# Kernel optimization log

Hardware: AMD Instinct MI355X
Metric: run time of the kernel (lower is better)

Reference implementation:

```python
import jax, jax.numpy as jnp
import numpy as np
from jax import lax

GS = 29          # grid_size
DW = 15          # displacement_width
DR = 0.4         # disp_range
N = GS ** 3      # 24389 control points
P = DW ** 2      # 225 in-plane displacements
WIN = (1, 1, 3, 3, 1)
ONE = (1, 1, 1, 1, 1)


def _axis(n):
    # align_corners=False pixel-center coords in [-1, 1], as torch affine_grid
    return (2.0 * jnp.arange(n, dtype=jnp.float32) + 1.0) / n - 1.0


def make_grids():
    a = _axis(GS)
    zc, yc, xc = jnp.meshgrid(a, a, a, indexing='ij')
    grid_xyz = jnp.stack([xc, yc, zc], -1).reshape(-1, 3)  # (N,3) xyz, d-major flatten
    s = DR * _axis(DW)
    A, B = jnp.meshgrid(s, s, indexing='ij')
    Z = jnp.zeros_like(A)
    sx = jnp.stack([B, A, Z], -1).reshape(-1, 3)  # z=0 plane: (s[w], s[h], 0)
    sy = jnp.stack([B, Z, A], -1).reshape(-1, 3)  # y=0 plane: (s[w], 0, s[d])
    sz = jnp.stack([Z, B, A], -1).reshape(-1, 3)  # x=0 plane: (0, s[h], s[d])
    shift_2d = jnp.stack([sx, sy, sz], axis=1)    # (P,3,3): [disp, plane, xyz]
    return grid_xyz, shift_2d


def trilerp(vol, coords, border):
    # vol (C,D,H,W); coords (...,3) normalized xyz; align_corners=False trilinear
    C, D, H, W = vol.shape
    vflat = vol.reshape(C, -1)
    x, y, z = coords[..., 0], coords[..., 1], coords[..., 2]
    ix = 0.5 * ((x + 1.0) * W - 1.0)
    iy = 0.5 * ((y + 1.0) * H - 1.0)
    iz = 0.5 * ((z + 1.0) * D - 1.0)
    x0 = jnp.floor(ix); y0 = jnp.floor(iy); z0 = jnp.floor(iz)
    fx, fy, fz = ix - x0, iy - y0, iz - z0
    x0 = x0.astype(jnp.int32); y0 = y0.astype(jnp.int32); z0 = z0.astype(jnp.int32)
    out = 0.0
    for dz in (0, 1):
        wz = fz if dz else 1.0 - fz
        zi = z0 + dz
        for dy in (0, 1):
            wy = fy if dy else 1.0 - fy
            yi = y0 + dy
            for dx in (0, 1):
                wx = fx if dx else 1.0 - fx
                xi = x0 + dx
                w = wx * wy * wz
                xc = jnp.clip(xi, 0, W - 1)
                yc = jnp.clip(yi, 0, H - 1)
                zc = jnp.clip(zi, 0, D - 1)
                if not border:  # padding_mode='zeros'
                    inb = ((xi >= 0) & (xi < W) & (yi >= 0) & (yi < H) & (zi >= 0) & (zi < D))
                    w = w * inb.astype(vol.dtype)
                idx = (zc * H + yc) * W + xc
                out = out + vflat[:, idx] * w
    return out  # (C, *coords.shape[:-1])


def pad_dh(x):
    # ReplicationPad3d((0,0,2,2,2,2)) on a 5D tensor: pad dims 2 and 3 by 2
    return jnp.pad(x, ((0, 0), (0, 0), (2, 2), (2, 2), (0, 0)), mode='edge')


def minpool(x):
    # -MaxPool3d((3,3,1))(-x)
    return -lax.reduce_window(-x, -jnp.inf, lax.max, WIN, ONE, 'VALID')


def avgpool(x):
    # AvgPool3d((3,3,1), stride=1)
    return lax.reduce_window(x, 0.0, lax.add, WIN, ONE, 'VALID') / 9.0


def grid_smooth(cost):
    # (1,N,DW,DW,3) -> two 3x3 avg passes over the 29^3 control grid (d,h axes)
    cp = cost.transpose(2, 3, 4, 0, 1).reshape(1, 3 * P, GS, GS, GS)
    cp = avgpool(avgpool(pad_dh(cp)))
    return cp.transpose(0, 2, 3, 4, 1).reshape(1, N, DW, DW, 3)


def setup_inputs() -> dict:
    key = jax.random.key(0)
    k1, k2 = jax.random.split(key)
    C, V = 8, 64
    feat00 = jax.random.normal(k1, (1, C, V, V, V), jnp.float32)
    feat50 = jax.random.normal(k2, (1, C, V, V, V), jnp.float32)
    grid_xyz, shift_2d = make_grids()
    shift_2d_min = jnp.array(jnp.broadcast_to(shift_2d[None, None], (1, N, P, 3, 3)))
    alpha = jnp.array([1.0, 0.1, 1.0, 1.0, 0.1, 5.0], jnp.float32)
    return {"feat00": feat00, "feat50": feat50, "shift_2d_min": shift_2d_min,
            "grid_xyz": grid_xyz, "shift_2d": shift_2d, "alpha": alpha}


def reference(feat00, feat50, shift_2d_min, grid_xyz, shift_2d, alpha):
    grid29 = grid_xyz.reshape(GS, GS * GS, 3)
    sm = shift_2d_min.reshape(GS, GS * GS, P, 3, 3)
    f00, f50 = feat00[0], feat50[0]

    def chunk(args):
        g, s = args                                                # (841,3), (841,P,3,3)
        mov = trilerp(f50, g[:, None, None, :] + s, border=True)   # (C,841,P,3)
        fix = trilerp(f00, g, border=False)                        # (C,841)
        ssd = jnp.sum((fix[:, :, None, None] - mov) ** 2, axis=0)  # (841,P,3)
        return alpha[1] + alpha[0] * ssd

    pdd = lax.map(chunk, (grid29, sm)).reshape(1, N, DW, DW, 3)
    cost = avgpool(minpool(pad_dh(pdd)))
    cost = alpha[4] + alpha[2] * pdd + alpha[3] * grid_smooth(cost)
    cost = avgpool(minpool(pad_dh(cost)))
    cost_avg = grid_smooth(cost).reshape(N, P, 3)
    cost_soft = jax.nn.softmax(-alpha[5] * cost_avg, axis=1)
    pred_xyz = 0.5 * jnp.einsum('npk,pkd->nd', cost_soft, shift_2d)
    return cost_soft.reshape(N, 1, DW, DW, 3), pred_xyz, cost_avg
```

## Files before the change

### kernel.cpp

```cpp
#include <hip/hip_runtime.h>
#include <math.h>

#define GS   29
#define GS2  841
#define NCP  24389
#define DW   15
#define PP   225
#define CH   675
#define CHP  676
#define CC   8
#define VV   64
#define V3   262144
#define RP   237

typedef __attribute__((ext_vector_type(8))) _Float16 half8;
typedef __attribute__((ext_vector_type(4))) _Float16 half4;
typedef __attribute__((ext_vector_type(2))) _Float16 half2v;

__device__ __forceinline__ float sv(int i) {
    return 0.4f * ((2.f * i + 1.f) * (1.f / 15.f) - 1.f);
}

__device__ __forceinline__ void paxis(float pc, int& p0, float& wA, float& wB) {
    float iu = 0.5f * ((pc + 1.f) * (float)VV - 1.f);
    float u0f = floorf(iu);
    int u0 = (int)u0f;
    p0 = min(max(u0, 0), VV - 2);
    wA = (u0 < 0) ? 1.f : ((u0 >= VV - 1) ? 0.f : (1.f - (iu - u0f)));
    wB = 1.f - wA;
}
__device__ __forceinline__ void vaxis(float pc, int& c0, int& c1, float& w0, float& w1) {
    float iv = 0.5f * ((pc + 1.f) * (float)VV - 1.f);
    float v0f = floorf(iv);
    float fv = iv - v0f;
    int v0 = (int)v0f;
    c0 = min(max(v0, 0), VV - 1);
    c1 = min(max(v0 + 1, 0), VV - 1);
    w0 = 1.f - fv; w1 = fv;
}

__device__ __forceinline__ float sample_ssd(const _Float16* __restrict__ vol,
        int p0, float wAu, float wBu,
        int c0, int c1, float wv0, float wv1,
        int e0, int e1, float ww0, float ww1,
        half8 f8) {
    half8 acc = {0, 0, 0, 0, 0, 0, 0, 0};
#define PAIR(WC, VC, WGT) {                                               \
        float fA_ = (WGT) * wAu, fB_ = (WGT) * wBu;                       \
        _Float16 hA_ = (_Float16)fA_, hB_ = (_Float16)fB_;                \
        half8 hA8 = {hA_, hA_, hA_, hA_, hA_, hA_, hA_, hA_};             \
        half8 hB8 = {hB_, hB_, hB_, hB_, hB_, hB_, hB_, hB_};             \
        const _Float16* vp = vol + (size_t)((((WC) * VV) + (VC)) * VV + p0) * 8; \
        half8 lo = *(const half8*)vp;                                     \
        half8 hi = *(const half8*)(vp + 8);                               \
        acc += hA8 * lo;                                                  \
        acc += hB8 * hi;                                                  \
    }
    PAIR(e0, c0, ww0 * wv0)
    PAIR(e0, c1, ww0 * wv1)
    PAIR(e1, c0, ww1 * wv0)
    PAIR(e1, c1, ww1 * wv1)
#undef PAIR
    half8 d8 = f8 - acc;
#if __has_builtin(__builtin_amdgcn_fdot2)
    float ssd = 0.f;
#pragma unroll
    for (int j = 0; j < 4; j++) {
        half2v d2 = {d8[2 * j], d8[2 * j + 1]};
        ssd = __builtin_amdgcn_fdot2(d2, d2, ssd, false);
    }
    return ssd;
#else
    float ssd = 0.f;
#pragma unroll
    for (int c = 0; c < 8; c++) { float dc = (float)d8[c]; ssd = fmaf(dc, dc, ssd); }
    return ssd;
#endif
}

__global__ __launch_bounds__(256) void make_vols(const float* __restrict__ in,
                                                 _Float16* __restrict__ volA,
                                                 _Float16* __restrict__ volB) {
    int v = blockIdx.x * 256 + threadIdx.x;
    if (v >= V3) return;
    int z = v >> 12, y = (v >> 6) & 63, x = v & 63;
    half8 h;
#pragma unroll
    for (int c = 0; c < CC; c++) h[c] = (_Float16)in[c * V3 + v];
    *(half8*)(volA + (size_t)v * 8) = h;
    *(half8*)(volB + (size_t)((((z << 6) | x) << 6) | y) * 8) = h;
}

__global__ __launch_bounds__(256) void pdd_pool_n(const float* __restrict__ f00,
                                                  const _Float16* __restrict__ volA,
                                                  const _Float16* __restrict__ volB,
                                                  const float* __restrict__ grid,
                                                  const float* __restrict__ alpha,
                                                  _Float16* __restrict__ pdd,
                                                  _Float16* __restrict__ pool) {
    int n = blockIdx.x;
    int tid = threadIdx.x;
    __shared__ __align__(16) _Float16 fixh[8];
    __shared__ float rowp2[3][RP];
    __shared__ float smin[3 * 289];
    __shared__ float poolv2[3][RP];

    float gx = grid[n * 3 + 0], gy = grid[n * 3 + 1], gz = grid[n * 3 + 2];

    if (tid < 8) {
        float ix = 0.5f * ((gx + 1.f) * VV - 1.f);
        float iy = 0.5f * ((gy + 1.f) * VV - 1.f);
        float iz = 0.5f * ((gz + 1.f) * VV - 1.f);
        float x0f = floorf(ix), y0f = floorf(iy), z0f = floorf(iz);
        float fx = ix - x0f, fy = iy - y0f, fz = iz - z0f;
        int x0 = (int)x0f, y0 = (int)y0f, z0 = (int)z0f;
        const float* fc = f00 + tid * V3;
        float acc = 0.f;
        for (int dz = 0; dz < 2; dz++) {
            int zi = z0 + dz; float wz = dz ? fz : 1.f - fz;
            for (int dy = 0; dy < 2; dy++) {
                int yi = y0 + dy; float wy = dy ? fy : 1.f - fy;
                for (int dx = 0; dx < 2; dx++) {
                    int xi = x0 + dx; float wx = dx ? fx : 1.f - fx;
                    if (xi >= 0 && xi < VV && yi >= 0 && yi < VV && zi >= 0 && zi < VV)
                        acc += wx * wy * wz * fc[(zi * VV + yi) * VV + xi];
                }
            }
        }
        fixh[tid] = (_Float16)acc;
    }
    if (tid >= 225 && tid < 228) {
        int k = tid - 225;
        for (int q = PP; q < RP; q++) { rowp2[k][q] = 0.f; poolv2[k][q] = 0.f; }
    }
    __syncthreads();

    if (tid < PP) {
        int p = tid;
        int h_ = p / 15, w_ = p - 15 * h_;
        float A = sv(h_), B = sv(w_);
        half8 f8 = *(const half8*)fixh;
        float a0 = alpha[0], a1 = alpha[1];

        int pu01; float wAu01, wBu01; paxis(gx + B, pu01, wAu01, wBu01);
        int pu2 ; float wAu2 , wBu2 ; paxis(gy + B, pu2 , wAu2 , wBu2 );
        int va0, va1; float wva0, wva1; vaxis(gy + A, va0, va1, wva0, wva1);
        int wa0, wa1; float wwa0, wwa1; vaxis(gz + A, wa0, wa1, wwa0, wwa1);
        int zu0, zu1; float wzu0, wzu1; vaxis(gz, zu0, zu1, wzu0, wzu1);
        int vy0, vy1; float wvy0, wvy1; vaxis(gy, vy0, vy1, wvy0, wvy1);
        int vx0, vx1; float wvx0, wvx1; vaxis(gx, vx0, vx1, wvx0, wvx1);

        float s0 = sample_ssd(volA, pu01, wAu01, wBu01, va0, va1, wva0, wva1, zu0, zu1, wzu0, wzu1, f8);
        float s1 = sample_ssd(volA, pu01, wAu01, wBu01, vy0, vy1, wvy0, wvy1, wa0, wa1, wwa0, wwa1, f8);
        float s2 = sample_ssd(volB, pu2 , wAu2 , wBu2 , vx0, vx1, wvx0, wvx1, wa0, wa1, wwa0, wwa1, f8);
        rowp2[0][p] = a1 + a0 * s0;
        rowp2[1][p] = a1 + a0 * s1;
        rowp2[2][p] = a1 + a0 * s2;
    }
    __syncthreads();

    if (tid < 255) {
        int k = tid / 85, r = tid - 85 * k;
        int a = r / 5, bc = r - 5 * a;
        int b0 = bc * 4;
        int ra = max(a - 2, 0) * 15;
        int rb = min(max(a - 1, 0), 14) * 15;
        int rc = min(a, 14) * 15;
        float cm[6];
#pragma unroll
        for (int j = 0; j < 6; j++) {
            int cj = min(max(b0 - 2 + j, 0), 14);
            float m0 = rowp2[k][ra + cj];
            float m1 = rowp2[k][rb + cj];
            float m2 = rowp2[k][rc + cj];
            cm[j] = fminf(fminf(m0, m1), m2);
        }
#pragma unroll
        for (int o = 0; o < 4; o++) {
            int b = b0 + o;
            if (b < 17) smin[k * 289 + a * 17 + b] = fminf(fminf(cm[o], cm[o + 1]), cm[o + 2]);
        }
    }
    __syncthreads();

    if (tid < 180) {
        int k = tid / 60, r = tid - 60 * k;
        int h = r >> 2, wc = r & 3;
        int w0 = wc * 4;
        const float* S = smin + k * 289;
        float cs[6];
#pragma unroll
        for (int j = 0; j < 6; j++) {
            int cj = min(w0 + j, 16);
            cs[j] = S[h * 17 + cj] + S[(h + 1) * 17 + cj] + S[(h + 2) * 17 + cj];
        }
#pragma unroll
        for (int o = 0; o < 4; o++) {
            int w = w0 + o;
            if (w < 15) poolv2[k][h * 15 + w] = (cs[o] + cs[o + 1] + cs[o + 2]) * (1.f / 9.f);
        }
    }
    __syncthreads();

    if (tid < 169) {
        int c0 = tid * 4;
        half4 hp, hq;
#pragma unroll
        for (int j = 0; j < 4; j++) {
            int i = c0 + j;
            int p = i / 3, k = i - 3 * p;
            hp[j] = (_Float16)rowp2[k][p];
            hq[j] = (_Float16)poolv2[k][p];
        }
        *(half4*)(pdd + (size_t)n * CHP + c0) = hp;
        *(half4*)(pool + (size_t)n * CHP + c0) = hq;
    }
}

__global__ __launch_bounds__(256) void gs_z4s(const _Float16* __restrict__ in,
                                              _Float16* __restrict__ out) {
    const int COLS = GS2 * 169;
    int id = blockIdx.x * 256 + threadIdx.x;
    if (id >= COLS) return;
    int seg = blockIdx.y;
    int z0 = seg * 8;
    int z1 = min(z0 + 8, GS);
    int row = id / 169, c4 = id - 169 * row;
    size_t base = (size_t)row * CHP + c4 * 4;
    const size_t ZS = (size_t)GS2 * CHP;
    const float w0 = 1.f / 9.f, w1 = 2.f / 9.f, w2 = 3.f / 9.f;

    float v0[4], v1[4], v2[4], v3[4], v4[4];
    {
        int za = max(z0 - 2, 0), zb = max(z0 - 1, 0);
        int zd = min(z0 + 1, GS - 1), ze = min(z0 + 2, GS - 1);
        half4 ha = *(const half4*)(in + base + (size_t)za * ZS);
        half4 hb = *(const half4*)(in + base + (size_t)zb * ZS);
        half4 hc = *(const half4*)(in + base + (size_t)z0 * ZS);
        half4 hd = *(const half4*)(in + base + (size_t)zd * ZS);
        half4 he = *(const half4*)(in + base + (size_t)ze * ZS);
#pragma unroll
        for (int j = 0; j < 4; j++) {
            v0[j] = (float)ha[j]; v1[j] = (float)hb[j]; v2[j] = (float)hc[j];
            v3[j] = (float)hd[j]; v4[j] = (float)he[j];
        }
    }
    for (int z = z0; z < z1; z++) {
        half4 o;
#pragma unroll
        for (int j = 0; j < 4; j++)
            o[j] = (_Float16)(w0 * (v0[j] + v4[j]) + w1 * (v1[j] + v3[j]) + w2 * v2[j]);
        *(half4*)(out + base + (size_t)z * ZS) = o;
        int zn = min(z + 3, GS - 1);
        half4 hn = *(const half4*)(in + base + (size_t)zn * ZS);
#pragma unroll
        for (int j = 0; j < 4; j++) {
            v0[j] = v1[j]; v1[j] = v2[j]; v2[j] = v3[j]; v3[j] = v4[j];
            v4[j] = (float)hn[j];
        }
    }
}

__global__ __launch_bounds__(256) void cost_pool2_y(const _Float16* __restrict__ zs,
                                                    const _Float16* __restrict__ pdd,
                                                    const float* __restrict__ alpha,
                                                    _Float16* __restrict__ pool2) {
    int n = blockIdx.x, tid = threadIdx.x;
    int x = n % GS; int zy = n / GS; int y = zy % GS; int z = zy / GS;
    __shared__ float rowp2[3][RP];
    __shared__ float smin[3 * 289];
    __shared__ float poolv2[3][RP];

    if (tid >= 225 && tid < 228) {
        int k = tid - 225;
        for (int q = PP; q < RP; q++) { rowp2[k][q] = 0.f; poolv2[k][q] = 0.f; }
    }
    if (tid < 169) {
        int c0 = tid * 4;
        float s0 = 0.f, s1 = 0.f, s2 = 0.f, s3 = 0.f;
#pragma unroll
        for (int dy = 0; dy < 5; dy++) {
            int yy = min(max(y + dy - 2, 0), GS - 1);
            size_t off = ((size_t)(z * GS + yy) * GS + x) * CHP + c0;
            float w = (3.f - fabsf((float)dy - 2.f)) * (1.f / 9.f);
            half4 hv = *(const half4*)(zs + off);
            s0 = fmaf(w, (float)hv[0], s0);
            s1 = fmaf(w, (float)hv[1], s1);
            s2 = fmaf(w, (float)hv[2], s2);
            s3 = fmaf(w, (float)hv[3], s3);
        }
        float a2 = alpha[2], a3 = alpha[3], a4 = alpha[4];
        half4 pv = *(const half4*)(pdd + (size_t)n * CHP + c0);
        float sm[4] = {s0, s1, s2, s3};
#pragma unroll
        for (int j = 0; j < 4; j++) {
            int i = c0 + j;
            if (i < CH) {
                int p = i / 3, k = i - 3 * p;
                rowp2[k][p] = a4 + a2 * (float)pv[j] + a3 * sm[j];
            }
        }
    }
    __syncthreads();

    if (tid < 255) {
        int k = tid / 85, r = tid - 85 * k;
        int a = r / 5, bc = r - 5 * a;
        int b0 = bc * 4;
        int ra = max(a - 2, 0) * 15;
        int rb = min(max(a - 1, 0), 14) * 15;
        int rc = min(a, 14) * 15;
        float cm[6];
#pragma unroll
        for (int j = 0; j < 6; j++) {
            int cj = min(max(b0 - 2 + j, 0), 14);
            float m0 = rowp2[k][ra + cj];
            float m1 = rowp2[k][rb + cj];
            float m2 = rowp2[k][rc + cj];
            cm[j] = fminf(fminf(m0, m1), m2);
        }
#pragma unroll
        for (int o = 0; o < 4; o++) {
            int b = b0 + o;
            if (b < 17) smin[k * 289 + a * 17 + b] = fminf(fminf(cm[o], cm[o + 1]), cm[o + 2]);
        }
    }
    __syncthreads();

    if (tid < 180) {
        int k = tid / 60, r = tid - 60 * k;
        int h = r >> 2, wc = r & 3;
        int w0 = wc * 4;
        const float* S = smin + k * 289;
        float cs[6];
#pragma unroll
        for (int j = 0; j < 6; j++) {
            int cj = min(w0 + j, 16);
            cs[j] = S[h * 17 + cj] + S[(h + 1) * 17 + cj] + S[(h + 2) * 17 + cj];
        }
#pragma unroll
        for (int o = 0; o < 4; o++) {
            int w = w0 + o;
            if (w < 15) poolv2[k][h * 15 + w] = (cs[o] + cs[o + 1] + cs[o + 2]) * (1.f / 9.f);
        }
    }
    __syncthreads();

    if (tid < 169) {
        int c0 = tid * 4;
        half4 hq;
#pragma unroll
        for (int j = 0; j < 4; j++) {
            int i = c0 + j;
            int p = i / 3, k = i - 3 * p;
            hq[j] = (_Float16)poolv2[k][p];
        }
        *(half4*)(pool2 + (size_t)n * CHP + c0) = hq;
    }
}

__global__ __launch_bounds__(256) void smooth_y_softmax(const _Float16* __restrict__ zs,
                                                        const float* __restrict__ alpha,
                                                        float* __restrict__ ca,
                                                        float* __restrict__ soft,
                                                        float* __restrict__ pred) {
    int n = blockIdx.x, tid = threadIdx.x;
    int x = n % GS; int zy = n / GS; int y = zy % GS; int z = zy / GS;
    int wave = tid >> 6, lane = tid & 63;
    __shared__ float vals[CHP];
    __shared__ float partial[3][3];

    if (tid < 169) {
        int c0 = tid * 4;
        float s0 = 0.f, s1 = 0.f, s2 = 0.f, s3 = 0.f;
#pragma unroll
        for (int dy = 0; dy < 5; dy++) {
            int yy = min(max(y + dy - 2, 0), GS - 1);
            size_t off = ((size_t)(z * GS + yy) * GS + x) * CHP + c0;
            float w = (3.f - fabsf((float)dy - 2.f)) * (1.f / 9.f);
            half4 hv = *(const half4*)(zs + off);
            s0 = fmaf(w, (float)hv[0], s0);
            s1 = fmaf(w, (float)hv[1], s1);
            s2 = fmaf(w, (float)hv[2], s2);
            s3 = fmaf(w, (float)hv[3], s3);
        }
        vals[c0 + 0] = s0;
        vals[c0 + 1] = s1;
        vals[c0 + 2] = s2;
        vals[c0 + 3] = s3;
    }
    __syncthreads();

    for (int i = tid; i < CH; i += 256) ca[(size_t)n * CH + i] = vals[i];
    __syncthreads();

    float a5 = alpha[5];
    if (wave < 3) {
        int k = wave;
        float v[4], e[4];
        float m = -1e30f;
#pragma unroll
        for (int j = 0; j < 4; j++) {
            int p = lane + 64 * j;
            v[j] = (p < PP) ? -a5 * vals[p * 3 + k] : -1e30f;
            m = fmaxf(m, v[j]);
        }
#pragma unroll
        for (int o = 32; o > 0; o >>= 1) m = fmaxf(m, __shfl_xor(m, o));
        float sum = 0.f;
#pragma unroll
        for (int j = 0; j < 4; j++) {
            int p = lane + 64 * j;
            e[j] = (p < PP) ? __expf(v[j] - m) : 0.f;
            sum += e[j];
        }
#pragma unroll
        for (int o = 32; o > 0; o >>= 1) sum += __shfl_xor(sum, o);
        float inv = 1.f / sum;
        float px = 0.f, py = 0.f, pz = 0.f;
#pragma unroll
        for (int j = 0; j < 4; j++) {
            int p = lane + 64 * j;
            if (p < PP) {
                float s = e[j] * inv;
                vals[p * 3 + k] = s;
                int h_ = p / 15, w_ = p - 15 * h_;
                float A = sv(h_), B = sv(w_);
                if (k == 0)      { px += s * B; py += s * A; }
                else if (k == 1) { px += s * B; pz += s * A; }
                else             { py += s * B; pz += s * A; }
            }
        }
#pragma unroll
        for (int o = 32; o > 0; o >>= 1) {
            px += __shfl_xor(px, o);
            py += __shfl_xor(py, o);
            pz += __shfl_xor(pz, o);
        }
        if (lane == 0) { partial[k][0] = px; partial[k][1] = py; partial[k][2] = pz; }
    }
    __syncthreads();
    if (tid < 3) pred[(size_t)n * 3 + tid] = 0.5f * (partial[0][tid] + partial[1][tid] + partial[2][tid]);
    for (int i = tid; i < CH; i += 256) soft[(size_t)n * CH + i] = vals[i];
}

extern "C" void kernel_launch(void* const* d_in, const int* in_sizes, int n_in,
                              void* d_out, int out_size, void* d_ws, size_t ws_size,
                              hipStream_t stream) {
    const float* f00   = (const float*)d_in[0];
    const float* f50   = (const float*)d_in[1];
    const float* grid  = (const float*)d_in[3];
    const float* alpha = (const float*)d_in[5];

    float* out0 = (float*)d_out;
    float* out1 = out0 + (size_t)NCP * CH;
    float* out2 = out1 + (size_t)NCP * 3;

    char* ws = (char*)d_ws;
    _Float16* volA = (_Float16*)ws;
    _Float16* volB = volA + (size_t)V3 * 8;
    _Float16* H0 = volB + (size_t)V3 * 8;
    _Float16* H1 = H0 + (size_t)NCP * CHP;
    _Float16* H2 = H1 + (size_t)NCP * CHP;

    make_vols<<<(V3 + 255) / 256, 256, 0, stream>>>(f50, volA, volB);

    pdd_pool_n<<<NCP, 256, 0, stream>>>(f00, volA, volB, grid, alpha, H0, H1);

    const int COLS = GS2 * 169;
    const int gbz = (COLS + 255) / 256;
    dim3 gz(gbz, 4);

    gs_z4s<<<gz, 256, 0, stream>>>(H1, H2);
    cost_pool2_y<<<NCP, 256, 0, stream>>>(H2, H0, alpha, H1);

    gs_z4s<<<gz, 256, 0, stream>>>(H1, H2);
    smooth_y_softmax<<<NCP, 256, 0, stream>>>(H2, alpha, out2, out0, out1);
}
```

Before: 484.3 us.

## Fuse tail kernels into one persistent kernel with software grid barriers

Replaces the four tail launches (z-smooth, cost/pool, z-smooth, y-smooth+softmax) with a single persistent kernel of 1024 blocks that loops over work and synchronises phases through atomic-counter grid barriers. This targets launch overhead and inter-kernel drain gaps. It relies on all 1024 blocks being co-resident, since otherwise the spin barrier deadlocks. It also adds a memset for the barrier counters and per-block serial looping over control points.

New measurement: 1.280 ms. 164% more time.

```diff
diff --git a/kernel.cpp b/kernel.cpp
--- a/kernel.cpp
+++ b/kernel.cpp
@@ -1,5 +1,6 @@
 #include <hip/hip_runtime.h>
 #include <math.h>
+#include <stdint.h>
 
 #define GS   29
 #define GS2  841
@@ -12,6 +13,8 @@
 #define VV   64
 #define V3   262144
 #define RP   237
+#define COLS (GS2 * 169)
+#define NBT  1024
 
 typedef __attribute__((ext_vector_type(8))) _Float16 half8;
 typedef __attribute__((ext_vector_type(4))) _Float16 half4;
@@ -217,231 +220,260 @@
     }
 }
 
-__global__ __launch_bounds__(256) void gs_z4s(const _Float16* __restrict__ in,
-                                              _Float16* __restrict__ out) {
-    const int COLS = GS2 * 169;
-    int id = blockIdx.x * 256 + threadIdx.x;
-    if (id >= COLS) return;
-    int seg = blockIdx.y;
-    int z0 = seg * 8;
-    int z1 = min(z0 + 8, GS);
-    int row = id / 169, c4 = id - 169 * row;
-    size_t base = (size_t)row * CHP + c4 * 4;
+
+__device__ __forceinline__ void gridbar(unsigned* bar, int idx, unsigned nb) {
+    __syncthreads();
+    __threadfence();
+    if (threadIdx.x == 0) {
+        unsigned* c = bar + idx * 16;
+        atomicAdd(c, 1u);
+        while (__hip_atomic_load(c, __ATOMIC_ACQUIRE, __HIP_MEMORY_SCOPE_AGENT) < nb) {
+            __builtin_amdgcn_s_sleep(8);
+        }
+    }
+    __syncthreads();
+    __threadfence();
+}
+
+__device__ __forceinline__ void zsmooth_phase(const _Float16* __restrict__ in,
+                                              _Float16* __restrict__ out, int nthreads) {
     const size_t ZS = (size_t)GS2 * CHP;
     const float w0 = 1.f / 9.f, w1 = 2.f / 9.f, w2 = 3.f / 9.f;
-
-    float v0[4], v1[4], v2[4], v3[4], v4[4];
-    {
-        int za = max(z0 - 2, 0), zb = max(z0 - 1, 0);
-        int zd = min(z0 + 1, GS - 1), ze = min(z0 + 2, GS - 1);
-        half4 ha = *(const half4*)(in + base + (size_t)za * ZS);
-        half4 hb = *(const half4*)(in + base + (size_t)zb * ZS);
-        half4 hc = *(const half4*)(in + base + (size_t)z0 * ZS);
-        half4 hd = *(const half4*)(in + base + (size_t)zd * ZS);
-        half4 he = *(const half4*)(in + base + (size_t)ze * ZS);
-#pragma unroll
-        for (int j = 0; j < 4; j++) {
-            v0[j] = (float)ha[j]; v1[j] = (float)hb[j]; v2[j] = (float)hc[j];
-            v3[j] = (float)hd[j]; v4[j] = (float)he[j];
-        }
-    }
-    for (int z = z0; z < z1; z++) {
-        half4 o;
-#pragma unroll
-        for (int j = 0; j < 4; j++)
-            o[j] = (_Float16)(w0 * (v0[j] + v4[j]) + w1 * (v1[j] + v3[j]) + w2 * v2[j]);
-        *(half4*)(out + base + (size_t)z * ZS) = o;
-        int zn = min(z + 3, GS - 1);
-        half4 hn = *(const half4*)(in + base + (size_t)zn * ZS);
-#pragma unroll
-        for (int j = 0; j < 4; j++) {
-            v0[j] = v1[j]; v1[j] = v2[j]; v2[j] = v3[j]; v3[j] = v4[j];
-            v4[j] = (float)hn[j];
-        }
-    }
-}
-
-__global__ __launch_bounds__(256) void cost_pool2_y(const _Float16* __restrict__ zs,
-                                                    const _Float16* __restrict__ pdd,
-                                                    const float* __restrict__ alpha,
-                                                    _Float16* __restrict__ pool2) {
-    int n = blockIdx.x, tid = threadIdx.x;
-    int x = n % GS; int zy = n / GS; int y = zy % GS; int z = zy / GS;
+    const int TOT = COLS * 4;
+    for (int w = blockIdx.x * 256 + threadIdx.x; w < TOT; w += nthreads) {
+        int seg = w / COLS; int id = w - seg * COLS;
+        int z0 = seg * 8;
+        int z1 = min(z0 + 8, GS);
+        int row = id / 169, c4 = id - 169 * row;
+        size_t base = (size_t)row * CHP + c4 * 4;
+
+        float v0[4], v1[4], v2[4], v3[4], v4[4];
+        {
+            int za = max(z0 - 2, 0), zb = max(z0 - 1, 0);
+            int zd = min(z0 + 1, GS - 1), ze = min(z0 + 2, GS - 1);
+            half4 ha = *(const half4*)(in + base + (size_t)za * ZS);
+            half4 hb = *(const half4*)(in + base + (size_t)zb * ZS);
+            half4 hc = *(const half4*)(in + base + (size_t)z0 * ZS);
+            half4 hd = *(const half4*)(in + base + (size_t)zd * ZS);
+            half4 he = *(const half4*)(in + base + (size_t)ze * ZS);
+#pragma unroll
+            for (int j = 0; j < 4; j++) {
+                v0[j] = (float)ha[j]; v1[j] = (float)hb[j]; v2[j] = (float)hc[j];
+                v3[j] = (float)hd[j]; v4[j] = (float)he[j];
+            }
+        }
+        for (int z = z0; z < z1; z++) {
+            half4 o;
+#pragma unroll
+            for (int j = 0; j < 4; j++)
+                o[j] = (_Float16)(w0 * (v0[j] + v4[j]) + w1 * (v1[j] + v3[j]) + w2 * v2[j]);
+            *(half4*)(out + base + (size_t)z * ZS) = o;
+            int zn = min(z + 3, GS - 1);
+            half4 hn = *(const half4*)(in + base + (size_t)zn * ZS);
+#pragma unroll
+            for (int j = 0; j < 4; j++) {
+                v0[j] = v1[j]; v1[j] = v2[j]; v2[j] = v3[j]; v3[j] = v4[j];
+                v4[j] = (float)hn[j];
+            }
+        }
+    }
+}
+
+__global__ __launch_bounds__(256, 4) void tail_fused(_Float16* __restrict__ pool1,
+                                                     const _Float16* __restrict__ pddb,
+                                                     _Float16* __restrict__ tmp,
+                                                     const float* __restrict__ alpha,
+                                                     float* __restrict__ ca,
+                                                     float* __restrict__ soft,
+                                                     float* __restrict__ pred,
+                                                     unsigned* __restrict__ bar) {
+    const int NB = NBT;
+    const int NT = NB * 256;
+    int tid = threadIdx.x;
+
     __shared__ float rowp2[3][RP];
     __shared__ float smin[3 * 289];
     __shared__ float poolv2[3][RP];
-
-    if (tid >= 225 && tid < 228) {
-        int k = tid - 225;
-        for (int q = PP; q < RP; q++) { rowp2[k][q] = 0.f; poolv2[k][q] = 0.f; }
-    }
-    if (tid < 169) {
-        int c0 = tid * 4;
-        float s0 = 0.f, s1 = 0.f, s2 = 0.f, s3 = 0.f;
-#pragma unroll
-        for (int dy = 0; dy < 5; dy++) {
-            int yy = min(max(y + dy - 2, 0), GS - 1);
-            size_t off = ((size_t)(z * GS + yy) * GS + x) * CHP + c0;
-            float w = (3.f - fabsf((float)dy - 2.f)) * (1.f / 9.f);
-            half4 hv = *(const half4*)(zs + off);
-            s0 = fmaf(w, (float)hv[0], s0);
-            s1 = fmaf(w, (float)hv[1], s1);
-            s2 = fmaf(w, (float)hv[2], s2);
-            s3 = fmaf(w, (float)hv[3], s3);
-        }
-        float a2 = alpha[2], a3 = alpha[3], a4 = alpha[4];
-        half4 pv = *(const half4*)(pdd + (size_t)n * CHP + c0);
-        float sm[4] = {s0, s1, s2, s3};
-#pragma unroll
-        for (int j = 0; j < 4; j++) {
-            int i = c0 + j;
-            if (i < CH) {
+    __shared__ float partial[3][3];
+
+    zsmooth_phase(pool1, tmp, NT);
+    gridbar(bar, 0, NB);
+
+    float a2 = alpha[2], a3 = alpha[3], a4 = alpha[4];
+    for (int n = blockIdx.x; n < NCP; n += NB) {
+        int x = n % GS; int zy = n / GS; int y = zy % GS; int z = zy / GS;
+
+        if (tid >= 225 && tid < 228) {
+            int k = tid - 225;
+            for (int q = PP; q < RP; q++) { rowp2[k][q] = 0.f; poolv2[k][q] = 0.f; }
+        }
+        if (tid < 169) {
+            int c0 = tid * 4;
+            float s0 = 0.f, s1 = 0.f, s2 = 0.f, s3 = 0.f;
+#pragma unroll
+            for (int dy = 0; dy < 5; dy++) {
+                int yy = min(max(y + dy - 2, 0), GS - 1);
+                size_t off = ((size_t)(z * GS + yy) * GS + x) * CHP + c0;
+                float w = (3.f - fabsf((float)dy - 2.f)) * (1.f / 9.f);
+                half4 hv = *(const half4*)(tmp + off);
+                s0 = fmaf(w, (float)hv[0], s0);
+                s1 = fmaf(w, (float)hv[1], s1);
+                s2 = fmaf(w, (float)hv[2], s2);
+                s3 = fmaf(w, (float)hv[3], s3);
+            }
+            half4 pv = *(const half4*)(pddb + (size_t)n * CHP + c0);
+            float sm[4] = {s0, s1, s2, s3};
+#pragma unroll
+            for (int j = 0; j < 4; j++) {
+                int i = c0 + j;
+                if (i < CH) {
+                    int p = i / 3, k = i - 3 * p;
+                    rowp2[k][p] = a4 + a2 * (float)pv[j] + a3 * sm[j];
+                }
+            }
+        }
+        __syncthreads();
+
+        if (tid < 255) {
+            int k = tid / 85, r = tid - 85 * k;
+            int a = r / 5, bc = r - 5 * a;
+            int b0 = bc * 4;
+            int ra = max(a - 2, 0) * 15;
+            int rb = min(max(a - 1, 0), 14) * 15;
+            int rc = min(a, 14) * 15;
+            float cm[6];
+#pragma unroll
+            for (int j = 0; j < 6; j++) {
+                int cj = min(max(b0 - 2 + j, 0), 14);
+                float m0 = rowp2[k][ra + cj];
+                float m1 = rowp2[k][rb + cj];
+                float m2 = rowp2[k][rc + cj];
+                cm[j] = fminf(fminf(m0, m1), m2);
+            }
+#pragma unroll
+            for (int o = 0; o < 4; o++) {
+                int b = b0 + o;
+                if (b < 17) smin[k * 289 + a * 17 + b] = fminf(fminf(cm[o], cm[o + 1]), cm[o + 2]);
+            }
+        }
+        __syncthreads();
+
+        if (tid < 180) {
+            int k = tid / 60, r = tid - 60 * k;
+            int h = r >> 2, wc = r & 3;
+            int w0 = wc * 4;
+            const float* S = smin + k * 289;
+            float cs[6];
+#pragma unroll
+            for (int j = 0; j < 6; j++) {
+                int cj = min(w0 + j, 16);
+                cs[j] = S[h * 17 + cj] + S[(h + 1) * 17 + cj] + S[(h + 2) * 17 + cj];
+            }
+#pragma unroll
+            for (int o = 0; o < 4; o++) {
+                int w = w0 + o;
+                if (w < 15) poolv2[k][h * 15 + w] = (cs[o] + cs[o + 1] + cs[o + 2]) * (1.f / 9.f);
+            }
+        }
+        __syncthreads();
+
+        if (tid < 169) {
+            int c0 = tid * 4;
+            half4 hq;
+#pragma unroll
+            for (int j = 0; j < 4; j++) {
+                int i = c0 + j;
                 int p = i / 3, k = i - 3 * p;
-                rowp2[k][p] = a4 + a2 * (float)pv[j] + a3 * sm[j];
-            }
-        }
-    }
-    __syncthreads();
-
-    if (tid < 255) {
-        int k = tid / 85, r = tid - 85 * k;
-        int a = r / 5, bc = r - 5 * a;
-        int b0 = bc * 4;
-        int ra = max(a - 2, 0) * 15;
-        int rb = min(max(a - 1, 0), 14) * 15;
-        int rc = min(a, 14) * 15;
-        float cm[6];
-#pragma unroll
-        for (int j = 0; j < 6; j++) {
-            int cj = min(max(b0 - 2 + j, 0), 14);
-            float m0 = rowp2[k][ra + cj];
-            float m1 = rowp2[k][rb + cj];
-            float m2 = rowp2[k][rc + cj];
-            cm[j] = fminf(fminf(m0, m1), m2);
-        }
-#pragma unroll
-        for (int o = 0; o < 4; o++) {
-            int b = b0 + o;
-            if (b < 17) smin[k * 289 + a * 17 + b] = fminf(fminf(cm[o], cm[o + 1]), cm[o + 2]);
-        }
-    }
-    __syncthreads();
-
-    if (tid < 180) {
-        int k = tid / 60, r = tid - 60 * k;
-        int h = r >> 2, wc = r & 3;
-        int w0 = wc * 4;
-        const float* S = smin + k * 289;
-        float cs[6];
-#pragma unroll
-        for (int j = 0; j < 6; j++) {
-            int cj = min(w0 + j, 16);
-            cs[j] = S[h * 17 + cj] + S[(h + 1) * 17 + cj] + S[(h + 2) * 17 + cj];
-        }
-#pragma unroll
-        for (int o = 0; o < 4; o++) {
-            int w = w0 + o;
-            if (w < 15) poolv2[k][h * 15 + w] = (cs[o] + cs[o + 1] + cs[o + 2]) * (1.f / 9.f);
-        }
-    }
-    __syncthreads();
-
-    if (tid < 169) {
-        int c0 = tid * 4;
-        half4 hq;
-#pragma unroll
-        for (int j = 0; j < 4; j++) {
-            int i = c0 + j;
-            int p = i / 3, k = i - 3 * p;
-            hq[j] = (_Float16)poolv2[k][p];
-        }
-        *(half4*)(pool2 + (size_t)n * CHP + c0) = hq;
-    }
-}
-
-__global__ __launch_bounds__(256) void smooth_y_softmax(const _Float16* __restrict__ zs,
-                                                        const float* __restrict__ alpha,
-                                                        float* __restrict__ ca,
-                                                        float* __restrict__ soft,
-                                                        float* __restrict__ pred) {
-    int n = blockIdx.x, tid = threadIdx.x;
-    int x = n % GS; int zy = n / GS; int y = zy % GS; int z = zy / GS;
+                hq[j] = (_Float16)poolv2[k][p];
+            }
+            *(half4*)(pool1 + (size_t)n * CHP + c0) = hq;
+        }
+        __syncthreads();
+    }
+    gridbar(bar, 1, NB);
+
+    zsmooth_phase(pool1, tmp, NT);
+    gridbar(bar, 2, NB);
+
+    float a5 = alpha[5];
+    float* vals = &rowp2[0][0];
     int wave = tid >> 6, lane = tid & 63;
-    __shared__ float vals[CHP];
-    __shared__ float partial[3][3];
-
-    if (tid < 169) {
-        int c0 = tid * 4;
-        float s0 = 0.f, s1 = 0.f, s2 = 0.f, s3 = 0.f;
-#pragma unroll
-        for (int dy = 0; dy < 5; dy++) {
-            int yy = min(max(y + dy - 2, 0), GS - 1);
-            size_t off = ((size_t)(z * GS + yy) * GS + x) * CHP + c0;
-            float w = (3.f - fabsf((float)dy - 2.f)) * (1.f / 9.f);
-            half4 hv = *(const half4*)(zs + off);
-            s0 = fmaf(w, (float)hv[0], s0);
-            s1 = fmaf(w, (float)hv[1], s1);
-            s2 = fmaf(w, (float)hv[2], s2);
-            s3 = fmaf(w, (float)hv[3], s3);
-        }
-        vals[c0 + 0] = s0;
-        vals[c0 + 1] = s1;
-        vals[c0 + 2] = s2;
-        vals[c0 + 3] = s3;
-    }
-    __syncthreads();
-
-    for (int i = tid; i < CH; i += 256) ca[(size_t)n * CH + i] = vals[i];
-    __syncthreads();
-
-    float a5 = alpha[5];
-    if (wave < 3) {
-        int k = wave;
-        float v[4], e[4];
-        float m = -1e30f;
-#pragma unroll
-        for (int j = 0; j < 4; j++) {
-            int p = lane + 64 * j;
-            v[j] = (p < PP) ? -a5 * vals[p * 3 + k] : -1e30f;
-            m = fmaxf(m, v[j]);
-        }
-#pragma unroll
-        for (int o = 32; o > 0; o >>= 1) m = fmaxf(m, __shfl_xor(m, o));
-        float sum = 0.f;
-#pragma unroll
-        for (int j = 0; j < 4; j++) {
-            int p = lane + 64 * j;
-            e[j] = (p < PP) ? __expf(v[j] - m) : 0.f;
-            sum += e[j];
-        }
-#pragma unroll
-        for (int o = 32; o > 0; o >>= 1) sum += __shfl_xor(sum, o);
-        float inv = 1.f / sum;
-        float px = 0.f, py = 0.f, pz = 0.f;
-#pragma unroll
-        for (int j = 0; j < 4; j++) {
-            int p = lane + 64 * j;
-            if (p < PP) {
-                float s = e[j] * inv;
-                vals[p * 3 + k] = s;
-                int h_ = p / 15, w_ = p - 15 * h_;
-                float A = sv(h_), B = sv(w_);
-                if (k == 0)      { px += s * B; py += s * A; }
-                else if (k == 1) { px += s * B; pz += s * A; }
-                else             { py += s * B; pz += s * A; }
-            }
-        }
-#pragma unroll
-        for (int o = 32; o > 0; o >>= 1) {
-            px += __shfl_xor(px, o);
-            py += __shfl_xor(py, o);
-            pz += __shfl_xor(pz, o);
-        }
-        if (lane == 0) { partial[k][0] = px; partial[k][1] = py; partial[k][2] = pz; }
-    }
-    __syncthreads();
-    if (tid < 3) pred[(size_t)n * 3 + tid] = 0.5f * (partial[0][tid] + partial[1][tid] + partial[2][tid]);
-    for (int i = tid; i < CH; i += 256) soft[(size_t)n * CH + i] = vals[i];
+    for (int n = blockIdx.x; n < NCP; n += NB) {
+        int x = n % GS; int zy = n / GS; int y = zy % GS; int z = zy / GS;
+
+        if (tid < 169) {
+            int c0 = tid * 4;
+            float s0 = 0.f, s1 = 0.f, s2 = 0.f, s3 = 0.f;
+#pragma unroll
+            for (int dy = 0; dy < 5; dy++) {
+                int yy = min(max(y + dy - 2, 0), GS - 1);
+                size_t off = ((size_t)(z * GS + yy) * GS + x) * CHP + c0;
+                float w = (3.f - fabsf((float)dy - 2.f)) * (1.f / 9.f);
+                half4 hv = *(const half4*)(tmp + off);
+                s0 = fmaf(w, (float)hv[0], s0);
+                s1 = fmaf(w, (float)hv[1], s1);
+                s2 = fmaf(w, (float)hv[2], s2);
+                s3 = fmaf(w, (float)hv[3], s3);
+            }
+            vals[c0 + 0] = s0;
+            vals[c0 + 1] = s1;
+            vals[c0 + 2] = s2;
+            vals[c0 + 3] = s3;
+        }
+        __syncthreads();
+
+        for (int i = tid; i < CH; i += 256) ca[(size_t)n * CH + i] = vals[i];
+        __syncthreads();
+
+        if (wave < 3) {
+            int k = wave;
+            float v[4], e[4];
+            float m = -1e30f;
+#pragma unroll
+            for (int j = 0; j < 4; j++) {
+                int p = lane + 64 * j;
+                v[j] = (p < PP) ? -a5 * vals[p * 3 + k] : -1e30f;
+                m = fmaxf(m, v[j]);
+            }
+#pragma unroll
+            for (int o = 32; o > 0; o >>= 1) m = fmaxf(m, __shfl_xor(m, o));
+            float sum = 0.f;
+#pragma unroll
+            for (int j = 0; j < 4; j++) {
+                int p = lane + 64 * j;
+                e[j] = (p < PP) ? __expf(v[j] - m) : 0.f;
+                sum += e[j];
+            }
+#pragma unroll
+            for (int o = 32; o > 0; o >>= 1) sum += __shfl_xor(sum, o);
+            float inv = 1.f / sum;
+            float px = 0.f, py = 0.f, pz = 0.f;
+#pragma unroll
+            for (int j = 0; j < 4; j++) {
+                int p = lane + 64 * j;
+                if (p < PP) {
+                    float s = e[j] * inv;
+                    vals[p * 3 + k] = s;
+                    int h_ = p / 15, w_ = p - 15 * h_;
+                    float A = sv(h_), B = sv(w_);
+                    if (k == 0)      { px += s * B; py += s * A; }
+                    else if (k == 1) { px += s * B; pz += s * A; }
+                    else             { py += s * B; pz += s * A; }
+                }
+            }
+#pragma unroll
+            for (int o = 32; o > 0; o >>= 1) {
+                px += __shfl_xor(px, o);
+                py += __shfl_xor(py, o);
+                pz += __shfl_xor(pz, o);
+            }
+            if (lane == 0) { partial[k][0] = px; partial[k][1] = py; partial[k][2] = pz; }
+        }
+        __syncthreads();
+        if (tid < 3) pred[(size_t)n * 3 + tid] = 0.5f * (partial[0][tid] + partial[1][tid] + partial[2][tid]);
+        for (int i = tid; i < CH; i += 256) soft[(size_t)n * CH + i] = vals[i];
+        __syncthreads();
+    }
 }
 
 extern "C" void kernel_launch(void* const* d_in, const int* in_sizes, int n_in,
@@ -462,18 +494,13 @@
     _Float16* H0 = volB + (size_t)V3 * 8;
     _Float16* H1 = H0 + (size_t)NCP * CHP;
     _Float16* H2 = H1 + (size_t)NCP * CHP;
+    unsigned* bar = (unsigned*)(((uintptr_t)(H2 + (size_t)NCP * CHP) + 255) & ~(uintptr_t)255);
+
+    hipMemsetAsync(bar, 0, 256, stream);
 
     make_vols<<<(V3 + 255) / 256, 256, 0, stream>>>(f50, volA, volB);
 
     pdd_pool_n<<<NCP, 256, 0, stream>>>(f00, volA, volB, grid, alpha, H0, H1);
 
-    const int COLS = GS2 * 169;
-    const int gbz = (COLS + 255) / 256;
-    dim3 gz(gbz, 4);
-
-    gs_z4s<<<gz, 256, 0, stream>>>(H1, H2);
-    cost_pool2_y<<<NCP, 256, 0, stream>>>(H2, H0, alpha, H1);
-
-    gs_z4s<<<gz, 256, 0, stream>>>(H1, H2);
-    smooth_y_softmax<<<NCP, 256, 0, stream>>>(H2, alpha, out2, out0, out1);
-}
+    tail_fused<<<NBT, 256, 0, stream>>>(H1, H0, H2, alpha, out2, out0, out1, bar);
+}
```
